# Kernel tuning notes

Hardware: AMD Instinct MI355X
Metric: run time of the kernel (lower is better)

## Reference

```python
import jax, jax.numpy as jnp
import numpy as np

SCALING = 2.0  # lora scaling attached via set_lora (lora_alpha / r)


def setup_inputs() -> dict:
    key = jax.random.key(0)
    ks = jax.random.split(key, 8)
    E, DIN, DOUT, N, K, R = 8, 2048, 2048, 4096, 2, 16
    inputs = jax.random.normal(ks[0], (N, DIN), jnp.float32)
    weight = jax.random.normal(ks[1], (E, DOUT, DIN), jnp.float32) * 0.02
    lora_A = jax.random.normal(ks[2], (E, R, DIN), jnp.float32) * 0.02
    lora_B = jax.random.normal(ks[3], (E, DOUT, R), jnp.float32) * 0.02
    gates = jax.nn.softmax(jax.random.normal(ks[4], (N, K), jnp.float32), axis=-1)
    # expert assignment per (token, slot); scattermoe contract:
    #   sorted_scattered_idxs = argsort(assign); token = idx // k, slot = idx % k
    assign = jax.random.randint(ks[5], (N * K,), 0, E)
    sorted_scattered_idxs = jnp.argsort(assign).astype(jnp.int32)
    sorted_expert_idxs = assign[sorted_scattered_idxs].astype(jnp.int32)
    counts = jnp.bincount(assign, length=E)
    expert_offsets = jnp.cumsum(counts).astype(jnp.int32)
    return dict(inputs=inputs, weight=weight, lora_A=lora_A, lora_B=lora_B,
                gates=gates, sorted_expert_idxs=sorted_expert_idxs,
                sorted_scattered_idxs=sorted_scattered_idxs,
                expert_offsets=expert_offsets, k=K)


def reference(inputs, weight, lora_A, lora_B, gates, sorted_expert_idxs,
              sorted_scattered_idxs, expert_offsets, k):
    # Fused LoRA grouped GEMM:  Y = X @ W + scaling * (X @ A^T) @ B^T
    # grouped_in=False, grouped_out=False, bias=None (module defaults).
    E = weight.shape[0]
    N = gates.shape[0]
    W = jnp.swapaxes(weight, 1, 2)          # [E, din, dout] (weight.permute(0,2,1))
    token = sorted_scattered_idxs // k      # source token per sorted slot
    slot = sorted_scattered_idxs % k        # which of the k routes
    x = inputs[token]                       # gather -> [N*k, din]
    y = jnp.zeros((x.shape[0], W.shape[2]), x.dtype)
    for e in range(E):                      # fixed small expert loop
        m = (sorted_expert_idxs == e)[:, None]
        xe = jnp.where(m, x, 0.0)
        y = y + (xe @ W[e] + SCALING * ((xe @ jnp.swapaxes(lora_A[e], 0, 1)) @ jnp.swapaxes(lora_B[e], 0, 1)))
    g = gates[token, slot][:, None]         # gate per sorted slot
    out = jnp.zeros((N, W.shape[2]), y.dtype).at[token].add(y * g)
    return out
```

## Files before the change

### kernel.cpp

```cpp
#include <hip/hip_runtime.h>
#include <hip/hip_bf16.h>

#define E_    8
#define DIN   2048
#define DOUT  2048
#define N_TOK 4096
#define NK    8192
#define R_    16
#define KEXT  2112
#define KT_N  (KEXT / 64)

typedef __bf16 bf16x8 __attribute__((ext_vector_type(8)));
typedef float  f32x4  __attribute__((ext_vector_type(4)));
typedef unsigned short u16x8 __attribute__((ext_vector_type(8)));

static __device__ __forceinline__ void gld16(const void* g, void* l) {
  __builtin_amdgcn_global_load_lds(
      (const __attribute__((address_space(1))) unsigned int*)g,
      (__attribute__((address_space(3))) unsigned int*)l, 16, 0, 0);
}

static __device__ __forceinline__ unsigned short f2bfu(float f) {
  union { float f; unsigned int u; } v; v.f = f;
  unsigned int r = v.u + 0x7fffu + ((v.u >> 16) & 1u);
  return (unsigned short)(r >> 16);
}

__global__ void __launch_bounds__(64)
k_wconv(const float* __restrict__ w, const float* __restrict__ lb,
        unsigned short* __restrict__ wbe) {
  const long long row = blockIdx.x;
  const float4* src  = (const float4*)(w + row * DIN);
  const float4* lsrc = (const float4*)(lb + row * R_);
  ushort4* dst = (ushort4*)(wbe + row * KEXT);
  for (int u = threadIdx.x; u < KEXT / 4; u += 64) {
    float4 v;
    if (u < 512)       v = src[u];
    else if (u < 516)  v = lsrc[u - 512];
    else               v = make_float4(0.f, 0.f, 0.f, 0.f);
    ushort4 o;
    o.x = f2bfu(v.x); o.y = f2bfu(v.y); o.z = f2bfu(v.z); o.w = f2bfu(v.w);
    dst[u] = o;
  }
}

__global__ void k_aconv(const float* __restrict__ a, unsigned short* __restrict__ ab) {
  long long i = (long long)blockIdx.x * blockDim.x + threadIdx.x;
  float4 v = ((const float4*)a)[i];
  ushort4 o;
  o.x = f2bfu(v.x); o.y = f2bfu(v.y); o.z = f2bfu(v.z); o.w = f2bfu(v.w);
  ((ushort4*)ab)[i] = o;
}

__global__ void k_gather(const float* __restrict__ x, const int* __restrict__ ssi,
                         const float* __restrict__ gates, const int* __restrict__ kptr,
                         unsigned short* __restrict__ Xe, float* __restrict__ gate,
                         int* __restrict__ tok) {
  int s = blockIdx.x;
  int ssv = ssi[s];
  int kk = kptr[0];
  int t = ssv / kk, sl = ssv - t * kk;
  if (threadIdx.x == 0) { gate[s] = gates[t * kk + sl]; tok[s] = t; }
  const float4* src = (const float4*)(x + (long long)t * DIN);
  ushort4* dst = (ushort4*)(Xe + (long long)s * KEXT);
  for (int i = threadIdx.x; i < 512; i += 256) {
    float4 v = src[i];
    ushort4 o;
    o.x = f2bfu(v.x); o.y = f2bfu(v.y); o.z = f2bfu(v.z); o.w = f2bfu(v.w);
    dst[i] = o;
  }
  if (threadIdx.x < 12) {
    ushort4 z; z.x = z.y = z.z = z.w = 0;
    dst[516 + threadIdx.x] = z;
  }
}

__global__ void __launch_bounds__(64)
k_xa(unsigned short* __restrict__ Xe, const unsigned short* __restrict__ Ab,
     const int* __restrict__ eoff) {
  int tile = blockIdx.x;
  int off_prev = 0, e = -1, m_start = 0, m_end = 0, acc_t = 0;
#pragma unroll
  for (int i = 0; i < E_; i++) {
    int oe = eoff[i];
    int te = (oe - off_prev + 15) >> 4;
    if (e < 0 && tile < acc_t + te) {
      e = i; m_start = off_prev + (tile - acc_t) * 16; m_end = oe;
    }
    acc_t += te; off_prev = oe;
  }
  if (e < 0) return;
  const int lane = threadIdx.x;
  const int l15 = lane & 15, quad = lane >> 4;
  int arow = m_start + l15; if (arow >= m_end) arow = m_end - 1;
  const unsigned short* xp = Xe + (long long)arow * KEXT + quad * 8;
  const unsigned short* bp = Ab + ((long long)e * R_ + l15) * DIN + quad * 8;
  f32x4 acc = (f32x4){0.f, 0.f, 0.f, 0.f};
#pragma unroll 8
  for (int k0 = 0; k0 < DIN; k0 += 32) {
    bf16x8 a = *(const bf16x8*)(xp + k0);
    bf16x8 b = *(const bf16x8*)(bp + k0);
    acc = __builtin_amdgcn_mfma_f32_16x16x32_bf16(a, b, acc, 0, 0, 0);
  }
#pragma unroll
  for (int t = 0; t < 4; t++) {
    int slot = m_start + quad * 4 + t;
    if (slot < m_end)
      Xe[(long long)slot * KEXT + 2048 + l15] = f2bfu(2.0f * acc[t]);
  }
}

__global__ void __launch_bounds__(256)
k_gemm(const unsigned short* __restrict__ Xe, const unsigned short* __restrict__ Wbe,
       const float* __restrict__ gate, const int* __restrict__ tok,
       const int* __restrict__ eoff, float* __restrict__ out) {
  __shared__ alignas(16) unsigned short sAB[2 * 128 * 64];
  __shared__ float gs[128];
  __shared__ int   ts[128];

  const int id = blockIdx.x;
  const int xcd = id & 7, local = id >> 3;
  const int mt = local % 72;
  const int nt = (xcd << 1) | (local / 72);
  const int n_start = nt << 7;

  int off_prev = 0, e = -1, m_start = 0, m_end = 0, acc_t = 0;
#pragma unroll
  for (int i = 0; i < E_; i++) {
    int oe = eoff[i];
    int te = (oe - off_prev + 127) >> 7;
    if (e < 0 && mt < acc_t + te) {
      e = i; m_start = off_prev + (mt - acc_t) * 128; m_end = oe;
    }
    acc_t += te;
    off_prev = oe;
  }
  if (e < 0) return;

  const int tid = threadIdx.x;
  const int w = tid >> 6, lane = tid & 63;
  const int wm = w & 1, wn = w >> 1;
  const int quad = lane >> 4, l15 = lane & 15;

  if (tid < 128) {
    int gm = m_start + tid; if (gm >= m_end) gm = m_end - 1;
    gs[tid] = gate[gm];
    ts[tid] = tok[gm];
  }

  f32x4 acc[4][4];
#pragma unroll
  for (int mi = 0; mi < 4; mi++)
#pragma unroll
    for (int ni = 0; ni < 4; ni++)
      acc[mi][ni] = (f32x4){0.f, 0.f, 0.f, 0.f};

  const int srow = lane >> 3;
  const int scol = ((lane & 7) ^ srow) * 8;
  const unsigned short* Wbase = Wbe + (long long)e * DOUT * KEXT;

  for (int kt = 0; kt < KT_N; kt++) {
    const int k0 = kt * 64;
#pragma unroll
    for (int j = 0; j < 4; j++) {
      int c = w * 4 + j;
      int rt = c * 8 + srow;
      int ga = m_start + rt; if (ga >= m_end) ga = m_end - 1;
      gld16(Xe + (long long)ga * KEXT + k0 + scol, &sAB[c * 512 + lane * 8]);
      gld16(Wbase + (long long)(n_start + rt) * KEXT + k0 + scol,
            &sAB[8192 + c * 512 + lane * 8]);
    }
    __syncthreads();
#pragma unroll
    for (int ks = 0; ks < 2; ks++) {
      const int kx = (((ks << 2) | quad) ^ (l15 & 7)) << 3;
      bf16x8 af[4], bfr[4];
#pragma unroll
      for (int mi = 0; mi < 4; mi++)
        af[mi] = *(const bf16x8*)&sAB[(wm * 64 + mi * 16 + l15) * 64 + kx];
#pragma unroll
      for (int ni = 0; ni < 4; ni++)
        bfr[ni] = *(const bf16x8*)&sAB[8192 + (wn * 64 + ni * 16 + l15) * 64 + kx];
#pragma unroll
      for (int mi = 0; mi < 4; mi++)
#pragma unroll
        for (int ni = 0; ni < 4; ni++)
          acc[mi][ni] = __builtin_amdgcn_mfma_f32_16x16x32_bf16(
              af[mi], bfr[ni], acc[mi][ni], 0, 0, 0);
    }
    __syncthreads();
  }

#pragma unroll
  for (int ni = 0; ni < 4; ni++) {
    int n = n_start + wn * 64 + ni * 16 + l15;
#pragma unroll
    for (int mi = 0; mi < 4; mi++) {
#pragma unroll
      for (int t4 = 0; t4 < 4; t4++) {
        int row = wm * 64 + mi * 16 + quad * 4 + t4;
        if (m_start + row >= m_end) continue;
        float o = acc[mi][ni][t4] * gs[row];
        atomicAdd(out + (long long)ts[row] * DOUT + n, o);
      }
    }
  }
}

extern "C" void kernel_launch(void* const* d_in, const int* in_sizes, int n_in,
                              void* d_out, int out_size, void* d_ws, size_t ws_size,
                              hipStream_t stream) {
  (void)in_sizes; (void)n_in; (void)out_size; (void)ws_size;
  const float* inputs = (const float*)d_in[0];
  const float* weight = (const float*)d_in[1];
  const float* lora_A = (const float*)d_in[2];
  const float* lora_B = (const float*)d_in[3];
  const float* gates  = (const float*)d_in[4];
  const int* sei  = (const int*)d_in[5];
  const int* ssi  = (const int*)d_in[6];
  const int* eoff = (const int*)d_in[7];
  const int* kptr = (const int*)d_in[8];
  (void)sei;
  float* out = (float*)d_out;

  unsigned char* ws = (unsigned char*)d_ws;
  unsigned short* Wbe = (unsigned short*)ws;
  unsigned short* Xe  = (unsigned short*)(ws + 69206016);
  unsigned short* Ab  = (unsigned short*)(ws + 103809024);
  float* gate = (float*)(ws + 104333312);
  int*   tok  = (int*)(ws + 104366080);

  hipMemsetAsync(d_out, 0, (size_t)N_TOK * DOUT * sizeof(float), stream);
  k_wconv<<<E_ * DOUT, 64, 0, stream>>>(weight, lora_B, Wbe);
  k_aconv<<<256, 256, 0, stream>>>(lora_A, Ab);
  k_gather<<<NK, 256, 0, stream>>>(inputs, ssi, gates, kptr, Xe, gate, tok);
  k_xa<<<519, 64, 0, stream>>>(Xe, Ab, eoff);
  k_gemm<<<1152, 256, 0, stream>>>(Xe, Wbe, gate, tok, eoff, out);
}
```

Baseline: 436.2 us.

## Enlarge grouped GEMM tiles to 256x256 with double-buffered LDS staging

The expert GEMM moves from 128x128 tiles with 256 threads to 256x256 tiles with 512 threads and 8 waves, each wave computing 128x64. LDS is now double-buffered so the next K-slice is loaded while the current one runs through MFMA. The aim is more operand reuse per global load and hidden load latency. The LoRA-A bf16 conversion is also folded into the gather kernel, removing one launch. In exchange, the larger LDS footprint (about 130KB) likely allows only one block per CU, and the coarser grid of 320 blocks may leave a load-imbalanced tail.

```diff
diff --git a/kernel.cpp b/kernel.cpp
--- a/kernel.cpp
+++ b/kernel.cpp
@@ -9,10 +9,12 @@
 #define R_    16
 #define KEXT  2112
 #define KT_N  (KEXT / 64)
+#define BM    256
+#define BN    256
+#define MT_MAX 40
 
 typedef __bf16 bf16x8 __attribute__((ext_vector_type(8)));
 typedef float  f32x4  __attribute__((ext_vector_type(4)));
-typedef unsigned short u16x8 __attribute__((ext_vector_type(8)));
 
 static __device__ __forceinline__ void gld16(const void* g, void* l) {
   __builtin_amdgcn_global_load_lds(
@@ -44,19 +46,19 @@
   }
 }
 
-__global__ void k_aconv(const float* __restrict__ a, unsigned short* __restrict__ ab) {
-  long long i = (long long)blockIdx.x * blockDim.x + threadIdx.x;
-  float4 v = ((const float4*)a)[i];
-  ushort4 o;
-  o.x = f2bfu(v.x); o.y = f2bfu(v.y); o.z = f2bfu(v.z); o.w = f2bfu(v.w);
-  ((ushort4*)ab)[i] = o;
-}
-
 __global__ void k_gather(const float* __restrict__ x, const int* __restrict__ ssi,
                          const float* __restrict__ gates, const int* __restrict__ kptr,
                          unsigned short* __restrict__ Xe, float* __restrict__ gate,
-                         int* __restrict__ tok) {
+                         int* __restrict__ tok,
+                         const float* __restrict__ la, unsigned short* __restrict__ Ab) {
   int s = blockIdx.x;
+  int ai = (s << 8) + threadIdx.x;
+  if (ai < (E_ * R_ * DIN / 4)) {
+    float4 v = ((const float4*)la)[ai];
+    ushort4 o;
+    o.x = f2bfu(v.x); o.y = f2bfu(v.y); o.z = f2bfu(v.z); o.w = f2bfu(v.w);
+    ((ushort4*)Ab)[ai] = o;
+  }
   int ssv = ssi[s];
   int kk = kptr[0];
   int t = ssv / kk, sl = ssv - t * kk;
@@ -110,27 +112,29 @@
   }
 }
 
-__global__ void __launch_bounds__(256)
+__global__ void __launch_bounds__(512, 2)
 k_gemm(const unsigned short* __restrict__ Xe, const unsigned short* __restrict__ Wbe,
        const float* __restrict__ gate, const int* __restrict__ tok,
        const int* __restrict__ eoff, float* __restrict__ out) {
-  __shared__ alignas(16) unsigned short sAB[2 * 128 * 64];
-  __shared__ float gs[128];
-  __shared__ int   ts[128];
-
-  const int id = blockIdx.x;
-  const int xcd = id & 7, local = id >> 3;
-  const int mt = local % 72;
-  const int nt = (xcd << 1) | (local / 72);
-  const int n_start = nt << 7;
+  __shared__ alignas(16) unsigned short sA[2][BM * 64];
+  __shared__ alignas(16) unsigned short sB[2][BN * 64];
+  __shared__ float gs[BM];
+  __shared__ int   ts[BM];
+
+  const int id  = blockIdx.x;
+  const int xcd = id & 7;
+  const int jb  = id >> 3;
+  const int nt  = jb & 7;
+  const int mt  = ((jb >> 3) << 3) | xcd;
+  const int n_start = nt << 8;
 
   int off_prev = 0, e = -1, m_start = 0, m_end = 0, acc_t = 0;
 #pragma unroll
   for (int i = 0; i < E_; i++) {
     int oe = eoff[i];
-    int te = (oe - off_prev + 127) >> 7;
+    int te = (oe - off_prev + 255) >> 8;
     if (e < 0 && mt < acc_t + te) {
-      e = i; m_start = off_prev + (mt - acc_t) * 128; m_end = oe;
+      e = i; m_start = off_prev + (mt - acc_t) * 256; m_end = oe;
     }
     acc_t += te;
     off_prev = oe;
@@ -139,50 +143,58 @@
 
   const int tid = threadIdx.x;
   const int w = tid >> 6, lane = tid & 63;
-  const int wm = w & 1, wn = w >> 1;
+  const int wm = w >> 2, wn = w & 3;
   const int quad = lane >> 4, l15 = lane & 15;
-
-  if (tid < 128) {
+  const int srow = lane >> 3;
+  const int scol = ((lane & 7) ^ srow) * 8;
+
+  if (tid < 256) {
     int gm = m_start + tid; if (gm >= m_end) gm = m_end - 1;
     gs[tid] = gate[gm];
     ts[tid] = tok[gm];
   }
 
-  f32x4 acc[4][4];
-#pragma unroll
-  for (int mi = 0; mi < 4; mi++)
+  f32x4 acc[8][4];
+#pragma unroll
+  for (int mi = 0; mi < 8; mi++)
 #pragma unroll
     for (int ni = 0; ni < 4; ni++)
       acc[mi][ni] = (f32x4){0.f, 0.f, 0.f, 0.f};
 
-  const int srow = lane >> 3;
-  const int scol = ((lane & 7) ^ srow) * 8;
-  const unsigned short* Wbase = Wbe + (long long)e * DOUT * KEXT;
+  const unsigned short* Wb = Wbe + (long long)e * DOUT * KEXT;
+
+#define STAGE(buf, kt_)                                                              \
+  {                                                                                  \
+    const int k0s = (kt_) * 64;                                                      \
+    _Pragma("unroll")                                                                \
+    for (int jj = 0; jj < 4; jj++) {                                                 \
+      const int c = (w << 2) + jj;                                                   \
+      const int rt = (c << 3) + srow;                                                \
+      int ga = m_start + rt; if (ga >= m_end) ga = m_end - 1;     \
+      gld16(Xe + (long long)ga * KEXT + k0s + scol, &sA[buf][(c << 9) + (lane << 3)]); \
+      gld16(Wb + (long long)(n_start + rt) * KEXT + k0s + scol,                      \
+            &sB[buf][(c << 9) + (lane << 3)]);                                       \
+    }                                                                                \
+  }
+
+  STAGE(0, 0);
+  __syncthreads();
 
   for (int kt = 0; kt < KT_N; kt++) {
-    const int k0 = kt * 64;
-#pragma unroll
-    for (int j = 0; j < 4; j++) {
-      int c = w * 4 + j;
-      int rt = c * 8 + srow;
-      int ga = m_start + rt; if (ga >= m_end) ga = m_end - 1;
-      gld16(Xe + (long long)ga * KEXT + k0 + scol, &sAB[c * 512 + lane * 8]);
-      gld16(Wbase + (long long)(n_start + rt) * KEXT + k0 + scol,
-            &sAB[8192 + c * 512 + lane * 8]);
-    }
-    __syncthreads();
+    const int b = kt & 1;
+    if (kt + 1 < KT_N) STAGE(b ^ 1, kt + 1);
 #pragma unroll
     for (int ks = 0; ks < 2; ks++) {
       const int kx = (((ks << 2) | quad) ^ (l15 & 7)) << 3;
-      bf16x8 af[4], bfr[4];
-#pragma unroll
-      for (int mi = 0; mi < 4; mi++)
-        af[mi] = *(const bf16x8*)&sAB[(wm * 64 + mi * 16 + l15) * 64 + kx];
+      bf16x8 af[8], bfr[4];
+#pragma unroll
+      for (int mi = 0; mi < 8; mi++)
+        af[mi] = *(const bf16x8*)&sA[b][(wm * 128 + mi * 16 + l15) * 64 + kx];
 #pragma unroll
       for (int ni = 0; ni < 4; ni++)
-        bfr[ni] = *(const bf16x8*)&sAB[8192 + (wn * 64 + ni * 16 + l15) * 64 + kx];
-#pragma unroll
-      for (int mi = 0; mi < 4; mi++)
+        bfr[ni] = *(const bf16x8*)&sB[b][(wn * 64 + ni * 16 + l15) * 64 + kx];
+#pragma unroll
+      for (int mi = 0; mi < 8; mi++)
 #pragma unroll
         for (int ni = 0; ni < 4; ni++)
           acc[mi][ni] = __builtin_amdgcn_mfma_f32_16x16x32_bf16(
@@ -190,19 +202,20 @@
     }
     __syncthreads();
   }
-
-#pragma unroll
-  for (int ni = 0; ni < 4; ni++) {
-    int n = n_start + wn * 64 + ni * 16 + l15;
-#pragma unroll
-    for (int mi = 0; mi < 4; mi++) {
-#pragma unroll
-      for (int t4 = 0; t4 < 4; t4++) {
-        int row = wm * 64 + mi * 16 + quad * 4 + t4;
-        if (m_start + row >= m_end) continue;
-        float o = acc[mi][ni][t4] * gs[row];
-        atomicAdd(out + (long long)ts[row] * DOUT + n, o);
-      }
+#undef STAGE
+
+#pragma unroll
+  for (int mi = 0; mi < 8; mi++) {
+    const int rbase = wm * 128 + mi * 16 + quad * 4;
+#pragma unroll
+    for (int t4 = 0; t4 < 4; t4++) {
+      const int row = rbase + t4;
+      if (m_start + row >= m_end) continue;
+      const float g = gs[row];
+      float* orow = out + (long long)ts[row] * DOUT + n_start + wn * 64 + l15;
+#pragma unroll
+      for (int ni = 0; ni < 4; ni++)
+        atomicAdd(orow + ni * 16, acc[mi][ni][t4] * g);
     }
   }
 }
@@ -232,8 +245,7 @@
 
   hipMemsetAsync(d_out, 0, (size_t)N_TOK * DOUT * sizeof(float), stream);
   k_wconv<<<E_ * DOUT, 64, 0, stream>>>(weight, lora_B, Wbe);
-  k_aconv<<<256, 256, 0, stream>>>(lora_A, Ab);
-  k_gather<<<NK, 256, 0, stream>>>(inputs, ssi, gates, kptr, Xe, gate, tok);
+  k_gather<<<NK, 256, 0, stream>>>(inputs, ssi, gates, kptr, Xe, gate, tok, lora_A, Ab);
   k_xa<<<519, 64, 0, stream>>>(Xe, Ab, eoff);
-  k_gemm<<<1152, 256, 0, stream>>>(Xe, Wbe, gate, tok, eoff, out);
-}
+  k_gemm<<<MT_MAX * 8, 512, 0, stream>>>(Xe, Wbe, gate, tok, eoff, out);
+}
```

After: 442.7 us. About the same (+1.5%).
